# Kernel optimization log

Measured on AMD Instinct MI355X. Metric: run time of the kernel, lower is better.

## Reference

```python
import jax, jax.numpy as jnp
import numpy as np

B, N, K = 1024, 200, 32
HID = 36
IN_DIM = K * (K + 2)  # k + q + flattened outer product


def setup_inputs() -> dict:
    key = jax.random.key(0)
    ks = jax.random.split(key, 4)
    candidate_ad = jax.random.normal(ks[0], (B, K), dtype=jnp.float32)
    goods = jax.random.normal(ks[1], (B, N, K), dtype=jnp.float32)
    W1 = jax.random.normal(ks[2], (IN_DIM, HID), dtype=jnp.float32) * (1.0 / np.sqrt(IN_DIM))
    b1 = jnp.zeros((HID,), dtype=jnp.float32)
    W2 = jax.random.normal(ks[3], (HID, 1), dtype=jnp.float32) * (1.0 / np.sqrt(HID))
    b2 = jnp.zeros((1,), dtype=jnp.float32)
    return {"candidate_ad": candidate_ad, "goods": goods, "W1": W1, "b1": b1, "W2": W2, "b2": b2}


def reference(candidate_ad, goods, W1, b1, W2, b2):
    # candidate_ad: [B, K] (attention key k), goods: [B, N, K] (queries q per item)
    Bs, Ns, Ks = goods.shape
    # outer product per item: einsum('bi,bj->bij', k, q) vectorized over N -> [B, N, K, K]
    outer = jnp.einsum('bi,bnj->bnij', candidate_ad, goods).reshape(Bs, Ns, Ks * Ks)
    k_b = jnp.broadcast_to(candidate_ad[:, None, :], (Bs, Ns, Ks))
    h1 = jnp.concatenate((k_b, goods, outer), axis=-1)          # [B, N, K*(K+2)]
    act = jax.nn.sigmoid(h1 @ W1 + b1)                           # [B, N, HID]
    weight = act @ W2 + b2                                       # [B, N, 1]
    out = jnp.sum(goods * weight, axis=1)                        # [B, K]
    return out
```

## Files before the change

kernel.cpp:

```cpp
#include <hip/hip_runtime.h>


#define BB 1024
#define BPB 2
#define NN 200
#define KK 32
#define HID 36
#define QP 40
#define LOG2E 1.44269504f

typedef __attribute__((ext_vector_type(8))) short bf16x8;
typedef __attribute__((ext_vector_type(4))) float f32x4;

__device__ __forceinline__ float rfl(float x) {
    return __uint_as_float(__builtin_amdgcn_readfirstlane(__float_as_uint(x)));
}
__device__ __forceinline__ unsigned short f2bf(float x) {
    unsigned int u = __float_as_uint(x);
    u = (u + 0x7fffu + ((u >> 16) & 1u)) >> 16;
    return (unsigned short)u;
}
__device__ __forceinline__ unsigned int pk_bf16(float lo, float hi) {
    unsigned int r;
    asm("v_cvt_pk_bf16_f32 %0, %1, %2" : "=v"(r) : "v"(lo), "v"(hi));
    return r;
}
__device__ __forceinline__ float fast_rcp(float x) {
#if __has_builtin(__builtin_amdgcn_rcpf)
    return __builtin_amdgcn_rcpf(x);
#else
    return 1.0f / x;
#endif
}
__device__ __forceinline__ float fast_exp2(float x) {
#if __has_builtin(__builtin_amdgcn_exp2f)
    return __builtin_amdgcn_exp2f(x);
#else
    return exp2f(x);
#endif
}

__global__ __launch_bounds__(512, 4) void din_kernel(
    const float* __restrict__ cad,
    const float* __restrict__ goods,
    const float* __restrict__ W1,
    const float* __restrict__ b1p,
    const float* __restrict__ W2,
    const float* __restrict__ b2p,
    float* __restrict__ out)
{
    __shared__ alignas(16) unsigned short V16[BPB][48 * QP];
    __shared__ alignas(16) float c48[BPB * 48];
    __shared__ alignas(16) float w248[48];
    __shared__ alignas(16) float red_s[BPB * 8 * KK];

    const int tid  = threadIdx.x;
    const int b0   = blockIdx.x * BPB;
    const int lane = tid & 63;
    const int wv   = tid >> 6;
    const int l15  = lane & 15, lk = lane >> 4;

    const float* gb0 = goods + (size_t)b0 * NN * KK;
    const float* gb1 = gb0 + (size_t)NN * KK;
    const float* k0p = cad + b0 * KK;
    const float* k1p = k0p + KK;

    const int rowm = [] (int r) { return r; } (0);
    float4 f0q0a, f0q0b, f1q0a, f1q0b;
    {
        const int r0 = (wv * 16 + l15) * KK + lk * 8;
        const float4* qp0 = reinterpret_cast<const float4*>(gb0 + r0);
        const float4* qp1 = reinterpret_cast<const float4*>(gb1 + r0);
        f0q0a = qp0[0]; f0q0b = qp0[1];
        f1q0a = qp1[0]; f1q0b = qp1[1];
    }
    float4 f0q1a = make_float4(0.f, 0.f, 0.f, 0.f), f0q1b = f0q1a;
    float4 f1q1a = f0q1a, f1q1b = f0q1a;
    if (wv < 5) {
        int row = (wv + 8) * 16 + l15;
        row = (row < NN) ? row : (NN - 1);
        const float4* qp0 = reinterpret_cast<const float4*>(gb0 + row * KK + lk * 8);
        const float4* qp1 = reinterpret_cast<const float4*>(gb1 + row * KK + lk * 8);
        f0q1a = qp0[0]; f0q1b = qp0[1];
        f1q1a = qp1[0]; f1q1b = qp1[1];
    }

    const float b2v = rfl(b2p[0]);

    const float4* W1q = reinterpret_cast<const float4*>(W1);
    if (tid < 288) {
        float4 acc0 = W1q[288 + tid];
        float4 acc1 = acc0;
        #pragma unroll 8
        for (int i = 0; i < KK; ++i) {
            const float ki0 = k0p[i];
            const float ki1 = k1p[i];
            const float4 w0 = W1q[576 + 288 * i + tid];
            acc0.x += ki0 * w0.x; acc0.y += ki0 * w0.y;
            acc0.z += ki0 * w0.z; acc0.w += ki0 * w0.w;
            acc1.x += ki1 * w0.x; acc1.y += ki1 * w0.y;
            acc1.z += ki1 * w0.z; acc1.w += ki1 * w0.w;
        }
        const float a0[4] = {acc0.x, acc0.y, acc0.z, acc0.w};
        const float a1[4] = {acc1.x, acc1.y, acc1.z, acc1.w};
        #pragma unroll
        for (int q = 0; q < 4; ++q) {
            const int e = 4 * tid + q, j = e / 36, h = e - 36 * j;
            V16[0][h * QP + j] = f2bf(a0[q]);
            V16[1][h * QP + j] = f2bf(a1[q]);
        }
    } else if (tid < 306) {
        const int u = tid - 288, bl = u / 9, hq = u % 9;
        const float* kp = bl ? k1p : k0p;
        float4 acc = reinterpret_cast<const float4*>(b1p)[hq];
        #pragma unroll 8
        for (int i = 0; i < KK; ++i) {
            const float ki = kp[i];
            const float4 wc = W1q[i * 9 + hq];
            acc.x += ki * wc.x; acc.y += ki * wc.y;
            acc.z += ki * wc.z; acc.w += ki * wc.w;
        }
        float4 cp4;
        cp4.x = -acc.x * LOG2E; cp4.y = -acc.y * LOG2E;
        cp4.z = -acc.z * LOG2E; cp4.w = -acc.w * LOG2E;
        *reinterpret_cast<float4*>(&c48[bl * 48 + 4 * hq]) = cp4;
    } else if (tid < 498) {
        const int r = tid - 306;
        const int w = (36 + (r >> 4)) * (QP / 2) + (r & 15);
        reinterpret_cast<unsigned int*>(V16[0])[w] = 0u;
        reinterpret_cast<unsigned int*>(V16[1])[w] = 0u;
    } else if (tid < 504) {
        const int u = tid - 498, bl = u / 3, q = u % 3;
        *reinterpret_cast<float4*>(&c48[bl * 48 + 36 + 4 * q]) =
            make_float4(0.f, 0.f, 0.f, 0.f);
    } else {
        const int u = tid - 504;
        *reinterpret_cast<float4*>(&w248[4 * u]) =
            reinterpret_cast<const float4*>(W2)[u];
        if (u == 0)
            *reinterpret_cast<float4*>(&w248[32]) =
                reinterpret_cast<const float4*>(W2)[8];
        else if (u < 4)
            *reinterpret_cast<float4*>(&w248[36 + 4 * (u - 1)]) =
                make_float4(0.f, 0.f, 0.f, 0.f);
    }
    __syncthreads();

    float facc0[8] = {0.f, 0.f, 0.f, 0.f, 0.f, 0.f, 0.f, 0.f};
    float facc1[8] = {0.f, 0.f, 0.f, 0.f, 0.f, 0.f, 0.f, 0.f};

    auto tile = [&](const float4& qa, const float4& qb, const bf16x8* bfr,
                    const float* cb, int m, bool masked, float* fa) {
        union { unsigned int u[4]; bf16x8 v; } aq;
        aq.u[0] = pk_bf16(qa.x, qa.y);
        aq.u[1] = pk_bf16(qa.z, qa.w);
        aq.u[2] = pk_bf16(qb.x, qb.y);
        aq.u[3] = pk_bf16(qb.z, qb.w);
        const f32x4 zero = {0.f, 0.f, 0.f, 0.f};
        const f32x4 d0 = __builtin_amdgcn_mfma_f32_16x16x32_bf16(bfr[0], aq.v, zero, 0, 0, 0);
        const f32x4 d1 = __builtin_amdgcn_mfma_f32_16x16x32_bf16(bfr[1], aq.v, zero, 0, 0, 0);
        const f32x4 d2 = __builtin_amdgcn_mfma_f32_16x16x32_bf16(bfr[2], aq.v, zero, 0, 0, 0);

        const f32x4 c0 = *reinterpret_cast<const f32x4*>(cb + lk * 4);
        const f32x4 w0 = *reinterpret_cast<const f32x4*>(&w248[lk * 4]);
        const f32x4 c1 = *reinterpret_cast<const f32x4*>(cb + 16 + lk * 4);
        const f32x4 w1 = *reinterpret_cast<const f32x4*>(&w248[16 + lk * 4]);
        const f32x4 c2 = *reinterpret_cast<const f32x4*>(cb + 32 + lk * 4);
        const f32x4 w2 = *reinterpret_cast<const f32x4*>(&w248[32 + lk * 4]);

        float p = 0.f;
        #pragma unroll
        for (int r = 0; r < 4; ++r) {
            p += fast_rcp(1.0f + fast_exp2(__builtin_fmaf(d0[r], -LOG2E, c0[r]))) * w0[r];
            p += fast_rcp(1.0f + fast_exp2(__builtin_fmaf(d1[r], -LOG2E, c1[r]))) * w1[r];
            p += fast_rcp(1.0f + fast_exp2(__builtin_fmaf(d2[r], -LOG2E, c2[r]))) * w2[r];
        }
        p += __shfl_xor(p, 16, 64);
        p += __shfl_xor(p, 32, 64);

        float wn = b2v + p;
        if (masked) {
            const int n = m * 16 + l15;
            wn = (n < NN) ? wn : 0.f;
        }
        fa[0] += qa.x * wn; fa[1] += qa.y * wn;
        fa[2] += qa.z * wn; fa[3] += qa.w * wn;
        fa[4] += qb.x * wn; fa[5] += qb.y * wn;
        fa[6] += qb.z * wn; fa[7] += qb.w * wn;
    };

    {
        bf16x8 bfr[3];
        #pragma unroll
        for (int nt = 0; nt < 3; ++nt)
            bfr[nt] = *reinterpret_cast<const bf16x8*>(&V16[0][(nt * 16 + l15) * QP + lk * 8]);
        tile(f0q0a, f0q0b, bfr, c48, wv, false, facc0);
        if (wv < 5) tile(f0q1a, f0q1b, bfr, c48, wv + 8, true, facc0);
    }
    {
        bf16x8 bfr[3];
        #pragma unroll
        for (int nt = 0; nt < 3; ++nt)
            bfr[nt] = *reinterpret_cast<const bf16x8*>(&V16[1][(nt * 16 + l15) * QP + lk * 8]);
        tile(f1q0a, f1q0b, bfr, c48 + 48, wv, false, facc1);
        if (wv < 5) tile(f1q1a, f1q1b, bfr, c48 + 48, wv + 8, true, facc1);
    }

    #pragma unroll
    for (int s = 1; s <= 8; s <<= 1) {
        #pragma unroll
        for (int u = 0; u < 8; ++u) {
            facc0[u] += __shfl_xor(facc0[u], s, 64);
            facc1[u] += __shfl_xor(facc1[u], s, 64);
        }
    }
    if (l15 == 0) {
        #pragma unroll
        for (int u = 0; u < 8; ++u) {
            red_s[wv * KK + lk * 8 + u]       = facc0[u];
            red_s[256 + wv * KK + lk * 8 + u] = facc1[u];
        }
    }
    __syncthreads();

    if (tid < BPB * KK) {
        const int bl = tid >> 5, j = tid & 31;
        float s = 0.f;
        #pragma unroll
        for (int w = 0; w < 8; ++w) s += red_s[bl * 256 + w * KK + j];
        out[(b0 + bl) * KK + j] = s;
    }
}

extern "C" void kernel_launch(void* const* d_in, const int* in_sizes, int n_in,
                              void* d_out, int out_size, void* d_ws, size_t ws_size,
                              hipStream_t stream) {
    const float* cad   = (const float*)d_in[0];
    const float* goods = (const float*)d_in[1];
    const float* W1    = (const float*)d_in[2];
    const float* b1    = (const float*)d_in[3];
    const float* W2    = (const float*)d_in[4];
    const float* b2    = (const float*)d_in[5];
    float* outp = (float*)d_out;

    din_kernel<<<BB / BPB, 512, 0, stream>>>(cad, goods, W1, b1, W2, b2, outp);
}
```

Before: 18.95 us.

## Process four batches per 1024-thread block to amortize W1 projection

New measurement: 15.41 us. 1.23x faster.

```diff
diff --git a/kernel.cpp b/kernel.cpp
--- a/kernel.cpp
+++ b/kernel.cpp
@@ -2,7 +2,7 @@
 
 
 #define BB 1024
-#define BPB 2
+#define BPB 4
 #define NN 200
 #define KK 32
 #define HID 36
@@ -40,7 +40,7 @@
 #endif
 }
 
-__global__ __launch_bounds__(512, 4) void din_kernel(
+__global__ __launch_bounds__(1024, 4) void din_kernel(
     const float* __restrict__ cad,
     const float* __restrict__ goods,
     const float* __restrict__ W1,
@@ -52,68 +52,59 @@
     __shared__ alignas(16) unsigned short V16[BPB][48 * QP];
     __shared__ alignas(16) float c48[BPB * 48];
     __shared__ alignas(16) float w248[48];
-    __shared__ alignas(16) float red_s[BPB * 8 * KK];
+    __shared__ alignas(16) float red_s[16 * KK];
 
     const int tid  = threadIdx.x;
     const int b0   = blockIdx.x * BPB;
     const int lane = tid & 63;
     const int wv   = tid >> 6;
     const int l15  = lane & 15, lk = lane >> 4;
-
-    const float* gb0 = goods + (size_t)b0 * NN * KK;
-    const float* gb1 = gb0 + (size_t)NN * KK;
+    const int bsel = wv & 3;
+    const int mrow = wv >> 2;
+
+    const float* gbw = goods + (size_t)(b0 + bsel) * NN * KK;
     const float* k0p = cad + b0 * KK;
     const float* k1p = k0p + KK;
-
-    const int rowm = [] (int r) { return r; } (0);
-    float4 f0q0a, f0q0b, f1q0a, f1q0b;
-    {
-        const int r0 = (wv * 16 + l15) * KK + lk * 8;
-        const float4* qp0 = reinterpret_cast<const float4*>(gb0 + r0);
-        const float4* qp1 = reinterpret_cast<const float4*>(gb1 + r0);
-        f0q0a = qp0[0]; f0q0b = qp0[1];
-        f1q0a = qp1[0]; f1q0b = qp1[1];
-    }
-    float4 f0q1a = make_float4(0.f, 0.f, 0.f, 0.f), f0q1b = f0q1a;
-    float4 f1q1a = f0q1a, f1q1b = f0q1a;
-    if (wv < 5) {
-        int row = (wv + 8) * 16 + l15;
-        row = (row < NN) ? row : (NN - 1);
-        const float4* qp0 = reinterpret_cast<const float4*>(gb0 + row * KK + lk * 8);
-        const float4* qp1 = reinterpret_cast<const float4*>(gb1 + row * KK + lk * 8);
-        f0q1a = qp0[0]; f0q1b = qp0[1];
-        f1q1a = qp1[0]; f1q1b = qp1[1];
-    }
+    const float* k2p = k1p + KK;
+    const float* k3p = k2p + KK;
 
     const float b2v = rfl(b2p[0]);
 
     const float4* W1q = reinterpret_cast<const float4*>(W1);
     if (tid < 288) {
         float4 acc0 = W1q[288 + tid];
-        float4 acc1 = acc0;
-        #pragma unroll 8
+        float4 acc1 = acc0, acc2 = acc0, acc3 = acc0;
+        #pragma unroll 4
         for (int i = 0; i < KK; ++i) {
-            const float ki0 = k0p[i];
-            const float ki1 = k1p[i];
             const float4 w0 = W1q[576 + 288 * i + tid];
+            const float ki0 = k0p[i], ki1 = k1p[i], ki2 = k2p[i], ki3 = k3p[i];
             acc0.x += ki0 * w0.x; acc0.y += ki0 * w0.y;
             acc0.z += ki0 * w0.z; acc0.w += ki0 * w0.w;
             acc1.x += ki1 * w0.x; acc1.y += ki1 * w0.y;
             acc1.z += ki1 * w0.z; acc1.w += ki1 * w0.w;
+            acc2.x += ki2 * w0.x; acc2.y += ki2 * w0.y;
+            acc2.z += ki2 * w0.z; acc2.w += ki2 * w0.w;
+            acc3.x += ki3 * w0.x; acc3.y += ki3 * w0.y;
+            acc3.z += ki3 * w0.z; acc3.w += ki3 * w0.w;
         }
         const float a0[4] = {acc0.x, acc0.y, acc0.z, acc0.w};
         const float a1[4] = {acc1.x, acc1.y, acc1.z, acc1.w};
+        const float a2[4] = {acc2.x, acc2.y, acc2.z, acc2.w};
+        const float a3[4] = {acc3.x, acc3.y, acc3.z, acc3.w};
         #pragma unroll
         for (int q = 0; q < 4; ++q) {
             const int e = 4 * tid + q, j = e / 36, h = e - 36 * j;
-            V16[0][h * QP + j] = f2bf(a0[q]);
-            V16[1][h * QP + j] = f2bf(a1[q]);
-        }
-    } else if (tid < 306) {
+            const int o = h * QP + j;
+            V16[0][o] = f2bf(a0[q]);
+            V16[1][o] = f2bf(a1[q]);
+            V16[2][o] = f2bf(a2[q]);
+            V16[3][o] = f2bf(a3[q]);
+        }
+    } else if (tid < 324) {
         const int u = tid - 288, bl = u / 9, hq = u % 9;
-        const float* kp = bl ? k1p : k0p;
+        const float* kp = cad + (b0 + bl) * KK;
         float4 acc = reinterpret_cast<const float4*>(b1p)[hq];
-        #pragma unroll 8
+        #pragma unroll 4
         for (int i = 0; i < KK; ++i) {
             const float ki = kp[i];
             const float4 wc = W1q[i * 9 + hq];
@@ -124,33 +115,36 @@
         cp4.x = -acc.x * LOG2E; cp4.y = -acc.y * LOG2E;
         cp4.z = -acc.z * LOG2E; cp4.w = -acc.w * LOG2E;
         *reinterpret_cast<float4*>(&c48[bl * 48 + 4 * hq]) = cp4;
-    } else if (tid < 498) {
-        const int r = tid - 306;
-        const int w = (36 + (r >> 4)) * (QP / 2) + (r & 15);
-        reinterpret_cast<unsigned int*>(V16[0])[w] = 0u;
-        reinterpret_cast<unsigned int*>(V16[1])[w] = 0u;
-    } else if (tid < 504) {
-        const int u = tid - 498, bl = u / 3, q = u % 3;
+    } else if (tid < 336) {
+        const int u = tid - 324, bl = u / 3, q = u % 3;
         *reinterpret_cast<float4*>(&c48[bl * 48 + 36 + 4 * q]) =
             make_float4(0.f, 0.f, 0.f, 0.f);
-    } else {
-        const int u = tid - 504;
-        *reinterpret_cast<float4*>(&w248[4 * u]) =
-            reinterpret_cast<const float4*>(W2)[u];
-        if (u == 0)
-            *reinterpret_cast<float4*>(&w248[32]) =
-                reinterpret_cast<const float4*>(W2)[8];
-        else if (u < 4)
-            *reinterpret_cast<float4*>(&w248[36 + 4 * (u - 1)]) =
+    } else if (tid < 348) {
+        const int u = tid - 336;
+        if (u < 9)
+            *reinterpret_cast<float4*>(&w248[4 * u]) =
+                reinterpret_cast<const float4*>(W2)[u];
+        else
+            *reinterpret_cast<float4*>(&w248[36 + 4 * (u - 9)]) =
                 make_float4(0.f, 0.f, 0.f, 0.f);
+    } else if (tid < 732) {
+        const int p = tid - 348;
+        const int word = p % 192, pair = p / 192;
+        const int w = (36 + (word >> 4)) * (QP / 2) + (word & 15);
+        reinterpret_cast<unsigned int*>(V16[2 * pair + 0])[w] = 0u;
+        reinterpret_cast<unsigned int*>(V16[2 * pair + 1])[w] = 0u;
     }
     __syncthreads();
 
-    float facc0[8] = {0.f, 0.f, 0.f, 0.f, 0.f, 0.f, 0.f, 0.f};
-    float facc1[8] = {0.f, 0.f, 0.f, 0.f, 0.f, 0.f, 0.f, 0.f};
-
-    auto tile = [&](const float4& qa, const float4& qb, const bf16x8* bfr,
-                    const float* cb, int m, bool masked, float* fa) {
+    bf16x8 bfr[3];
+    #pragma unroll
+    for (int nt = 0; nt < 3; ++nt)
+        bfr[nt] = *reinterpret_cast<const bf16x8*>(&V16[bsel][(nt * 16 + l15) * QP + lk * 8]);
+    const float* cb = c48 + bsel * 48;
+
+    float facc[8] = {0.f, 0.f, 0.f, 0.f, 0.f, 0.f, 0.f, 0.f};
+
+    auto tile = [&](const float4& qa, const float4& qb, int m, bool masked) {
         union { unsigned int u[4]; bf16x8 v; } aq;
         aq.u[0] = pk_bf16(qa.x, qa.y);
         aq.u[1] = pk_bf16(qa.z, qa.w);
@@ -183,43 +177,33 @@
             const int n = m * 16 + l15;
             wn = (n < NN) ? wn : 0.f;
         }
-        fa[0] += qa.x * wn; fa[1] += qa.y * wn;
-        fa[2] += qa.z * wn; fa[3] += qa.w * wn;
-        fa[4] += qb.x * wn; fa[5] += qb.y * wn;
-        fa[6] += qb.z * wn; fa[7] += qb.w * wn;
+        facc[0] += qa.x * wn; facc[1] += qa.y * wn;
+        facc[2] += qa.z * wn; facc[3] += qa.w * wn;
+        facc[4] += qb.x * wn; facc[5] += qb.y * wn;
+        facc[6] += qb.z * wn; facc[7] += qb.w * wn;
     };
 
-    {
-        bf16x8 bfr[3];
-        #pragma unroll
-        for (int nt = 0; nt < 3; ++nt)
-            bfr[nt] = *reinterpret_cast<const bf16x8*>(&V16[0][(nt * 16 + l15) * QP + lk * 8]);
-        tile(f0q0a, f0q0b, bfr, c48, wv, false, facc0);
-        if (wv < 5) tile(f0q1a, f0q1b, bfr, c48, wv + 8, true, facc0);
-    }
-    {
-        bf16x8 bfr[3];
-        #pragma unroll
-        for (int nt = 0; nt < 3; ++nt)
-            bfr[nt] = *reinterpret_cast<const bf16x8*>(&V16[1][(nt * 16 + l15) * QP + lk * 8]);
-        tile(f1q0a, f1q0b, bfr, c48 + 48, wv, false, facc1);
-        if (wv < 5) tile(f1q1a, f1q1b, bfr, c48 + 48, wv + 8, true, facc1);
+    #pragma unroll
+    for (int t = 0; t < 4; ++t) {
+        const int m = mrow + 4 * t;
+        if (m < 13) {
+            int row = m * 16 + l15;
+            row = (row < NN) ? row : (NN - 1);
+            const float4* qp = reinterpret_cast<const float4*>(gbw + row * KK + lk * 8);
+            tile(qp[0], qp[1], m, m == 12);
+        }
     }
 
     #pragma unroll
     for (int s = 1; s <= 8; s <<= 1) {
         #pragma unroll
-        for (int u = 0; u < 8; ++u) {
-            facc0[u] += __shfl_xor(facc0[u], s, 64);
-            facc1[u] += __shfl_xor(facc1[u], s, 64);
-        }
+        for (int u = 0; u < 8; ++u)
+            facc[u] += __shfl_xor(facc[u], s, 64);
     }
     if (l15 == 0) {
         #pragma unroll
-        for (int u = 0; u < 8; ++u) {
-            red_s[wv * KK + lk * 8 + u]       = facc0[u];
-            red_s[256 + wv * KK + lk * 8 + u] = facc1[u];
-        }
+        for (int u = 0; u < 8; ++u)
+            red_s[(bsel * 4 + mrow) * KK + lk * 8 + u] = facc[u];
     }
     __syncthreads();
 
@@ -227,7 +211,7 @@
         const int bl = tid >> 5, j = tid & 31;
         float s = 0.f;
         #pragma unroll
-        for (int w = 0; w < 8; ++w) s += red_s[bl * 256 + w * KK + j];
+        for (int g = 0; g < 4; ++g) s += red_s[(bl * 4 + g) * KK + j];
         out[(b0 + bl) * KK + j] = s;
     }
 }
@@ -243,5 +227,5 @@
     const float* b2    = (const float*)d_in[5];
     float* outp = (float*)d_out;
 
-    din_kernel<<<BB / BPB, 512, 0, stream>>>(cad, goods, W1, b1, W2, b2, outp);
-}
+    din_kernel<<<BB / BPB, 1024, 0, stream>>>(cad, goods, W1, b1, W2, b2, outp);
+}
```
